# Optimization experiments

Hardware: AMD Instinct MI355X
Metric: run time of the kernel (lower is better)

The kernel has to match this reference:

```python
import jax, jax.numpy as jnp
import numpy as np

C = 256          # num_input_channels[-1]
D_REC = 256      # recog_feature_depth
B = 4            # regions (pages)
R = 1024         # boxes per region
N = B * R
T_REC = 16
K = 32           # self.k: 1 self slot + K-1 neighbors
D_MODEL = 256    # 2 * initial_depth
N_HEADS = 8
D_FF = 512
N_LAYERS = 4
SEM_DIM = 113    # initial_depth - 1 - pos_channels(14)
EPS = 1e-5


def _bn1d(x, g, b):
    # eval-mode BatchNorm, running mean 0 / var 1
    return x * (g / jnp.sqrt(1.0 + EPS)) + b


def _ln(x, g, b):
    m = x.mean(-1, keepdims=True)
    v = ((x - m) ** 2).mean(-1, keepdims=True)
    return (x - m) * jax.lax.rsqrt(v + EPS) * g + b


def _forward(rectified_quads, original_quads, recog_features,
             conv_w, conv_b, conv_bn_g, conv_bn_b,
             recog_w, recog_b,
             cp_w1, cp_b1, cp_bn1_g, cp_bn1_b,
             cp_w2, cp_b2, cp_bn2_g, cp_bn2_b,
             enc_wqkv, enc_bqkv, enc_wo, enc_bo,
             enc_ln1_g, enc_ln1_b, enc_ln2_g, enc_ln2_b,
             enc_w1, enc_b1, enc_w2, enc_b2,
             head_w, head_b, region_counts):
    n = rectified_quads.shape[0]
    b = region_counts.shape[0]
    r = n // b  # equal-size regions
    kn = K - 1

    quads = original_quads / 1024.0  # quad_downscale
    mid_pts = jax.lax.stop_gradient(quads.mean(axis=1))  # [N,2]

    # rect_proj: 1x1 conv + eval BN2d + ReLU, averaged over the 2x3 grid
    h = jnp.einsum('oc,nchw->nohw', conv_w, rectified_quads) + conv_b[None, :, None, None]
    h = jax.nn.relu(h * (conv_bn_g / jnp.sqrt(1.0 + EPS))[None, :, None, None] + conv_bn_b[None, :, None, None])
    avg_rects = h.reshape(n, C, -1).sum(axis=2) / 6.0  # num_valid_pos = g_w*g_h

    recog_enc = (jax.lax.stop_gradient(recog_features) @ recog_w.T + recog_b).mean(axis=1)

    sem = jnp.concatenate([avg_rects, recog_enc], axis=1)
    sem = jax.nn.relu(_bn1d(sem @ cp_w1.T + cp_b1, cp_bn1_g, cp_bn1_b))
    sem = jax.nn.relu(_bn1d(sem @ cp_w2.T + cp_b2, cp_bn2_g, cp_bn2_b))  # [N,113]

    h1 = quads[:, 3] - quads[:, 0]
    h2 = quads[:, 2] - quads[:, 1]
    d1 = (quads[:, 1] + h2 / 2) - (quads[:, 0] + h1 / 2)
    wdth = jnp.linalg.norm(d1, axis=1, keepdims=True)
    d1 = d1 / jnp.maximum(wdth, 1e-6)
    hts = jnp.linalg.norm((h1 + h2) / 2, axis=1, keepdims=True)
    d2 = jnp.stack([-d1[:, 1], d1[:, 0]], axis=-1)
    full_enc = jnp.concatenate([sem, quads.reshape(n, 8), d1, d2, wdth, hts], axis=1)  # [N,127]

    rects = full_enc.reshape(b, r, -1)
    centers = mid_pts.reshape(b, r, 2)
    qds = quads.reshape(b, r, 4, 2)

    def region(cr, cc, cq):
        # kNN by quad-center euclidean distance, self excluded
        qc = cq.mean(axis=1)  # [r,2]
        sq = ((qc[:, None] - qc[None, :]) ** 2).sum(-1)
        eye = jnp.eye(r, dtype=bool)
        dist = jnp.sqrt(jnp.where(eye, 1.0, sq))
        dist = jnp.where(eye, jnp.inf, dist)
        negd, idx = jax.lax.top_k(-dist, kn)  # kn smallest
        nd = -negd                             # [r,kn]
        to_rects = cr[idx]                     # [r,kn,127]
        to_centers = cc[idx]                   # [r,kn,2]

        # cosine direction features (detached in the original)
        cqs = jax.lax.stop_gradient(cq)
        tcs = jax.lax.stop_gradient(to_centers)
        pt0 = (cqs[:, 0] + cqs[:, 3]) / 2
        pt1 = (cqs[:, 1] + cqs[:, 2]) / 2
        dr = pt1 - pt0
        dr = dr / jnp.maximum(jnp.linalg.norm(dr, axis=1, keepdims=True), 1e-6)
        ctr = (pt0 + pt1) / 2
        vec = tcs - ctr[:, None]
        vec = vec / jnp.maximum(jnp.linalg.norm(vec, axis=2, keepdims=True), 1e-6)
        cosang = jnp.einsum('fv,ftv->ft', dr, vec)  # [r,kn]

        to_rects = jnp.concatenate([jnp.zeros((r, 1, to_rects.shape[-1]), to_rects.dtype), to_rects], axis=1)
        dists = jnp.concatenate([jnp.full((r, 1), -1.0, nd.dtype), nd], axis=1)
        dirs = jnp.concatenate([jnp.full((r, 1), -2.0, cosang.dtype), cosang], axis=1)
        to_feat = jnp.concatenate([to_rects, dists[..., None], dirs[..., None]], axis=2)  # [r,K,129]
        from_feat = jnp.broadcast_to(cr[:, None, :], (r, K, cr.shape[-1]))
        enc_in = jnp.concatenate([from_feat, to_feat], axis=2)  # [r,K,256]
        idx_full = jnp.concatenate([jnp.zeros((r, 1), idx.dtype), idx + 1], axis=1)  # [r,K]
        return enc_in, idx_full

    enc_in, idx_full = jax.vmap(region)(rects, centers, qds)

    # pre-norm TransformerEncoder (eval: no dropout) + Linear(dim, 3)
    x = enc_in.reshape(b * r, K, D_MODEL)
    dh = D_MODEL // N_HEADS
    for i in range(N_LAYERS):
        y = _ln(x, enc_ln1_g[i], enc_ln1_b[i])
        qkv = y @ enc_wqkv[i].T + enc_bqkv[i]
        q, k_, v = jnp.split(qkv, 3, axis=-1)
        q = q.reshape(-1, K, N_HEADS, dh).transpose(0, 2, 1, 3)
        k_ = k_.reshape(-1, K, N_HEADS, dh).transpose(0, 2, 1, 3)
        v = v.reshape(-1, K, N_HEADS, dh).transpose(0, 2, 1, 3)
        att = jax.nn.softmax(jnp.einsum('nhqd,nhkd->nhqk', q, k_) / jnp.sqrt(jnp.float32(dh)), axis=-1)
        o = jnp.einsum('nhqk,nhkd->nhqd', att, v).transpose(0, 2, 1, 3).reshape(-1, K, D_MODEL)
        x = x + o @ enc_wo[i].T + enc_bo[i]
        y = _ln(x, enc_ln2_g[i], enc_ln2_b[i])
        x = x + jax.nn.relu(y @ enc_w1[i].T + enc_b1[i]) @ enc_w2[i].T + enc_b2[i]
    dots = (x @ head_w.T + head_b).reshape(b, r, K, 3).transpose(0, 3, 1, 2)  # [b,3,r,K]

    # prohibit_self_connection: scatter into a -inf [r, r+1] relation matrix
    rows = jnp.arange(r)[:, None]

    def scat(dv, iv):
        out = jnp.full((3, r, r + 1), -jnp.inf, dv.dtype)
        return out.at[:, rows, iv].set(dv)

    # [b,3,r,r+1]: channel 0=words, 1=lines, 2=line_log_var_unc
    return jax.vmap(scat)(dots, idx_full)


def setup_inputs() -> dict:
    key = jax.random.key(0)
    ks = jax.random.split(key, 64)
    it = iter(range(64))

    def rn(shape, s=0.05):
        return jax.random.normal(ks[next(it)], shape, jnp.float32) * s

    inp = {}
    inp['rectified_quads'] = jax.random.normal(ks[next(it)], (N, C, 2, 3), jnp.float32)
    inp['original_quads'] = jax.random.uniform(ks[next(it)], (N, 4, 2), jnp.float32) * 1024.0
    inp['recog_features'] = jax.random.normal(ks[next(it)], (N, T_REC, D_REC), jnp.float32)
    inp['conv_w'] = rn((C, C)); inp['conv_b'] = rn((C,))
    inp['conv_bn_g'] = 1.0 + rn((C,)); inp['conv_bn_b'] = rn((C,))
    inp['recog_w'] = rn((C, D_REC)); inp['recog_b'] = rn((C,))
    inp['cp_w1'] = rn((2 * C, 2 * C)); inp['cp_b1'] = rn((2 * C,))
    inp['cp_bn1_g'] = 1.0 + rn((2 * C,)); inp['cp_bn1_b'] = rn((2 * C,))
    inp['cp_w2'] = rn((SEM_DIM, 2 * C)); inp['cp_b2'] = rn((SEM_DIM,))
    inp['cp_bn2_g'] = 1.0 + rn((SEM_DIM,)); inp['cp_bn2_b'] = rn((SEM_DIM,))
    L = N_LAYERS
    inp['enc_wqkv'] = rn((L, 3 * D_MODEL, D_MODEL)); inp['enc_bqkv'] = rn((L, 3 * D_MODEL))
    inp['enc_wo'] = rn((L, D_MODEL, D_MODEL)); inp['enc_bo'] = rn((L, D_MODEL))
    inp['enc_ln1_g'] = jnp.ones((L, D_MODEL)); inp['enc_ln1_b'] = jnp.zeros((L, D_MODEL))
    inp['enc_ln2_g'] = jnp.ones((L, D_MODEL)); inp['enc_ln2_b'] = jnp.zeros((L, D_MODEL))
    inp['enc_w1'] = rn((L, D_FF, D_MODEL)); inp['enc_b1'] = rn((L, D_FF))
    inp['enc_w2'] = rn((L, D_MODEL, D_FF)); inp['enc_b2'] = rn((L, D_MODEL))
    inp['head_w'] = rn((3, D_MODEL)); inp['head_b'] = rn((3,))
    inp['region_counts'] = jnp.full((B,), R, dtype=jnp.int32)
    return inp


def reference(rectified_quads, original_quads, recog_features,
              conv_w, conv_b, conv_bn_g, conv_bn_b,
              recog_w, recog_b,
              cp_w1, cp_b1, cp_bn1_g, cp_bn1_b,
              cp_w2, cp_b2, cp_bn2_g, cp_bn2_b,
              enc_wqkv, enc_bqkv, enc_wo, enc_bo,
              enc_ln1_g, enc_ln1_b, enc_ln2_g, enc_ln2_b,
              enc_w1, enc_b1, enc_w2, enc_b2,
              head_w, head_b, region_counts):
    return _forward(rectified_quads, original_quads, recog_features,
                    conv_w, conv_b, conv_bn_g, conv_bn_b,
                    recog_w, recog_b,
                    cp_w1, cp_b1, cp_bn1_g, cp_bn1_b,
                    cp_w2, cp_b2, cp_bn2_g, cp_bn2_b,
                    enc_wqkv, enc_bqkv, enc_wo, enc_bo,
                    enc_ln1_g, enc_ln1_b, enc_ln2_g, enc_ln2_b,
                    enc_w1, enc_b1, enc_w2, enc_b2,
                    head_w, head_b, region_counts)
```

## Files before the change

### kernel.cpp

```cpp
#include <hip/hip_runtime.h>
#include <cmath>

#define KN    31
#define EPSV  1e-5f
#define NEG_BIG -1.0e30f

typedef unsigned short u16;
typedef unsigned long long u64;
typedef __attribute__((ext_vector_type(8))) short bf16x8_t;
typedef __attribute__((ext_vector_type(4))) float f32x4_t;

#define LDS_FENCE() asm volatile("s_waitcnt lgkmcnt(0)" ::: "memory")

__device__ __forceinline__ u16 f2bf(float f) {
  unsigned u = __float_as_uint(f);
  u += 0x7fffu + ((u >> 16) & 1u);
  return (u16)(u >> 16);
}

__global__ void k_cvt(const float* __restrict__ src, u16* __restrict__ dst, int n) {
  int i = blockIdx.x * blockDim.x + threadIdx.x;
  if (i < n) dst[i] = f2bf(src[i]);
}

__global__ __launch_bounds__(256) void k_rect(const float* __restrict__ rq,
    const float* __restrict__ w, const float* __restrict__ cb,
    const float* __restrict__ g, const float* __restrict__ bb,
    float* __restrict__ concat) {
  __shared__ float xs[1536];
  int n = blockIdx.x, t = threadIdx.x;
  const float* src = rq + (size_t)n * 1536;
  for (int i = t; i < 1536; i += 256) xs[i] = src[i];
  __syncthreads();
  float acc[6] = {0, 0, 0, 0, 0, 0};
  const float* wr = w + (size_t)t * 256;
  for (int c = 0; c < 256; c++) {
    float wv = wr[c];
#pragma unroll
    for (int p = 0; p < 6; p++) acc[p] += wv * xs[c * 6 + p];
  }
  float scale = g[t] / sqrtf(1.f + EPSV);
  float sh = bb[t], cbv = cb[t];
  float s = 0.f;
#pragma unroll
  for (int p = 0; p < 6; p++) {
    float v = (acc[p] + cbv) * scale + sh;
    s += fmaxf(v, 0.f);
  }
  concat[(size_t)n * 512 + t] = s * (1.f / 6.f);
}

__global__ __launch_bounds__(256) void k_recog(const float* __restrict__ rf,
    const float* __restrict__ w, const float* __restrict__ b,
    float* __restrict__ concat) {
  __shared__ float tmp[256];
  int n = blockIdx.x, t = threadIdx.x;
  const float* src = rf + (size_t)n * 4096;
  float s = 0.f;
  for (int tt = 0; tt < 16; tt++) s += src[tt * 256 + t];
  tmp[t] = s * (1.f / 16.f);
  __syncthreads();
  const float* wr = w + (size_t)t * 256;
  float d = b[t];
  for (int c = 0; c < 256; c++) d += wr[c] * tmp[c];
  concat[(size_t)n * 512 + 256 + t] = d;
}

__global__ __launch_bounds__(256) void k_sem(const float* __restrict__ concat,
    const float* __restrict__ w1, const float* __restrict__ b1,
    const float* __restrict__ g1, const float* __restrict__ s1,
    const float* __restrict__ w2, const float* __restrict__ b2,
    const float* __restrict__ g2, const float* __restrict__ s2,
    float* __restrict__ fe) {
  __shared__ float in4[4][512];
  __shared__ float h1[4][512];
  int n0 = blockIdx.x * 4, t = threadIdx.x;
  for (int i = t; i < 2048; i += 256) in4[i >> 9][i & 511] = concat[(size_t)n0 * 512 + i];
  __syncthreads();
#pragma unroll
  for (int rep = 0; rep < 2; rep++) {
    int o = t + rep * 256;
    float a0 = 0, a1 = 0, a2 = 0, a3 = 0;
    const float* wr = w1 + (size_t)o * 512;
    for (int k = 0; k < 512; k++) {
      float wv = wr[k];
      a0 += wv * in4[0][k]; a1 += wv * in4[1][k];
      a2 += wv * in4[2][k]; a3 += wv * in4[3][k];
    }
    float sc = g1[o] / sqrtf(1.f + EPSV), sh = s1[o], bi = b1[o];
    h1[0][o] = fmaxf((a0 + bi) * sc + sh, 0.f);
    h1[1][o] = fmaxf((a1 + bi) * sc + sh, 0.f);
    h1[2][o] = fmaxf((a2 + bi) * sc + sh, 0.f);
    h1[3][o] = fmaxf((a3 + bi) * sc + sh, 0.f);
  }
  __syncthreads();
  if (t < 113) {
    const float* wr = w2 + (size_t)t * 512;
    float sc = g2[t] / sqrtf(1.f + EPSV), sh = s2[t], bi = b2[t];
    for (int bb = 0; bb < 4; bb++) {
      float a = 0.f;
      for (int k = 0; k < 512; k++) a += wr[k] * h1[bb][k];
      fe[(size_t)(n0 + bb) * 127 + t] = fmaxf((a + bi) * sc + sh, 0.f);
    }
  }
}

__global__ void k_geom(const float* __restrict__ oq, float* __restrict__ fe,
                       float* __restrict__ qc) {
  int n = blockIdx.x * blockDim.x + threadIdx.x;
  if (n >= 4096) return;
  const float* q = oq + (size_t)n * 8;
  float p[8];
#pragma unroll
  for (int i = 0; i < 8; i++) p[i] = q[i] * (1.f / 1024.f);
  float cx = __fadd_rn(__fadd_rn(__fadd_rn(p[0], p[2]), p[4]), p[6]) * 0.25f;
  float cy = __fadd_rn(__fadd_rn(__fadd_rn(p[1], p[3]), p[5]), p[7]) * 0.25f;
  qc[n * 2] = cx; qc[n * 2 + 1] = cy;
  float h1x = p[6] - p[0], h1y = p[7] - p[1];
  float h2x = p[4] - p[2], h2y = p[5] - p[3];
  float d1x = (p[2] + h2x * 0.5f) - (p[0] + h1x * 0.5f);
  float d1y = (p[3] + h2y * 0.5f) - (p[1] + h1y * 0.5f);
  float wd = sqrtf(d1x * d1x + d1y * d1y);
  float iw = 1.f / fmaxf(wd, 1e-6f);
  d1x *= iw; d1y *= iw;
  float mx = (h1x + h2x) * 0.5f, my = (h1y + h2y) * 0.5f;
  float ht = sqrtf(mx * mx + my * my);
  float* o = fe + (size_t)n * 127 + 113;
  o[0] = p[0]; o[1] = p[1]; o[2] = p[2]; o[3] = p[3];
  o[4] = p[4]; o[5] = p[5]; o[6] = p[6]; o[7] = p[7];
  o[8] = d1x; o[9] = d1y; o[10] = -d1y; o[11] = d1x;
  o[12] = wd; o[13] = ht;
}

__global__ __launch_bounds__(64) void k_knn(const float* __restrict__ qc,
    const float* __restrict__ oq,
    int* __restrict__ nidx, float* __restrict__ ndist, float* __restrict__ ncos) {
  int gb = blockIdx.x;
  int b = gb >> 10, fl = gb & 1023;
  int l = threadIdx.x;
  const float* qcr = qc + (size_t)b * 2048;
  const float2* qc2 = (const float2*)qcr;
  float fx = qcr[fl * 2], fy = qcr[fl * 2 + 1];
  u64 key[16];
#pragma unroll
  for (int m = 0; m < 16; m++) {
    int j = l + 64 * m;
    float2 c = qc2[j];
    float dx = __fsub_rn(fx, c.x);
    float dy = __fsub_rn(fy, c.y);
    float sq = __fadd_rn(__fmul_rn(dx, dx), __fmul_rn(dy, dy));
    float d = sqrtf(sq);
    key[m] = ((u64)__float_as_uint(d) << 32) | (unsigned)j;
    if (j == fl) key[m] = ~0ull;
  }
  unsigned my_idx = 0; float my_d = 0.f;
  for (int s = 0; s < KN; s++) {
    u64 mk = ~0ull; int mi = 0;
#pragma unroll
    for (int m = 0; m < 16; m++) if (key[m] < mk) { mk = key[m]; mi = m; }
    u64 rk = mk;
#pragma unroll
    for (int off = 1; off < 64; off <<= 1) {
      u64 o = __shfl_xor(rk, off);
      if (o < rk) rk = o;
    }
    if (mk == rk) key[mi] = ~0ull;
    if (s == l) { my_idx = (unsigned)(rk & 0xffffffffu); my_d = __uint_as_float((unsigned)(rk >> 32)); }
  }
  if (l < KN) {
    const float* q = oq + (size_t)gb * 8;
    float p0x = q[0] * (1.f / 1024.f), p0y = q[1] * (1.f / 1024.f);
    float p1x = q[2] * (1.f / 1024.f), p1y = q[3] * (1.f / 1024.f);
    float p2x = q[4] * (1.f / 1024.f), p2y = q[5] * (1.f / 1024.f);
    float p3x = q[6] * (1.f / 1024.f), p3y = q[7] * (1.f / 1024.f);
    float pt0x = (p0x + p3x) * 0.5f, pt0y = (p0y + p3y) * 0.5f;
    float pt1x = (p1x + p2x) * 0.5f, pt1y = (p1y + p2y) * 0.5f;
    float drx = pt1x - pt0x, dry = pt1y - pt0y;
    float dn = sqrtf(drx * drx + dry * dry);
    float idn = 1.f / fmaxf(dn, 1e-6f);
    drx *= idn; dry *= idn;
    float ctrx = (pt0x + pt1x) * 0.5f, ctry = (pt0y + pt1y) * 0.5f;
    float2 nc = qc2[my_idx];
    float vx = nc.x - ctrx, vy = nc.y - ctry;
    float nv = sqrtf(vx * vx + vy * vy);
    float inv = 1.f / fmaxf(nv, 1e-6f);
    ncos[(size_t)gb * KN + l] = drx * (vx * inv) + dry * (vy * inv);
    ndist[(size_t)gb * KN + l] = my_d;
    nidx[(size_t)gb * KN + l] = (int)my_idx;
  }
}

__global__ __launch_bounds__(256) void k_build(const float* __restrict__ fe,
    const int* __restrict__ nidx, const float* __restrict__ ndist,
    const float* __restrict__ ncos, float* __restrict__ x) {
  __shared__ float self[127];
  int f = blockIdx.x, t = threadIdx.x;
  if (t < 127) self[t] = fe[(size_t)f * 127 + t];
  __syncthreads();
  int base = f & ~1023;
  float* xr = x + (size_t)f * 32 * 256;
  for (int s = 0; s < 32; s++) {
    float v;
    if (t < 127) v = self[t];
    else if (t < 254) {
      int c = t - 127;
      if (s == 0) v = 0.f;
      else {
        int nb = base + nidx[(size_t)f * KN + s - 1];
        v = fe[(size_t)nb * 127 + c];
      }
    } else if (t == 254) v = (s == 0) ? -1.f : ndist[(size_t)f * KN + s - 1];
    else                 v = (s == 0) ? -2.f : ncos[(size_t)f * KN + s - 1];
    xr[s * 256 + t] = v;
  }
}

#define AFRS 520
__global__ __launch_bounds__(256, 2) void k_xf(
    float* __restrict__ x,
    const u16* __restrict__ wqkv_b, const float* __restrict__ bqkv,
    const u16* __restrict__ wo_b,  const float* __restrict__ bo,
    const float* __restrict__ l1g, const float* __restrict__ l1b,
    const float* __restrict__ l2g, const float* __restrict__ l2b,
    const u16* __restrict__ w1_b,  const float* __restrict__ b1,
    const u16* __restrict__ w2_b,  const float* __restrict__ b2) {
  __shared__ u16 afr[32 * AFRS];
  __shared__ union {
    u16 scr[4][2560];
    u16 mfr[32 * AFRS];
    float ores[64][132];
  } uu;
  int t = threadIdx.x;
  int w = t >> 6, l = t & 63;
  int ln15 = l & 15, lg4 = l >> 4;
  int r = t >> 3, c8 = t & 7;
  float* xg = x + (size_t)blockIdx.x * 64 * 256;

  float xv[2][32];
#pragma unroll
  for (int b = 0; b < 2; b++)
#pragma unroll
    for (int u4 = 0; u4 < 8; u4++) {
      float4 v4 = ((const float4*)(xg + (b * 32 + r) * 256 + c8 * 32))[u4];
      xv[b][u4 * 4 + 0] = v4.x; xv[b][u4 * 4 + 1] = v4.y;
      xv[b][u4 * 4 + 2] = v4.z; xv[b][u4 * 4 + 3] = v4.w;
    }

  const float iss = 0.17677669529663687f;

  auto ln_afr = [&](const float* gg, const float* bb) {
#pragma unroll
    for (int b = 0; b < 2; b++) {
      float s = 0.f, q = 0.f;
#pragma unroll
      for (int i = 0; i < 32; i++) { s += xv[b][i]; q += xv[b][i] * xv[b][i]; }
      s += __shfl_xor(s, 1); q += __shfl_xor(q, 1);
      s += __shfl_xor(s, 2); q += __shfl_xor(q, 2);
      s += __shfl_xor(s, 4); q += __shfl_xor(q, 4);
      float mean = s * (1.f / 256.f);
      float var = q * (1.f / 256.f) - mean * mean;
      float rstd = rsqrtf(fmaxf(var, 0.f) + EPSV);
      int k0 = c8 * 32;
      unsigned pk[16];
#pragma unroll
      for (int i2 = 0; i2 < 16; i2++) {
        float y0 = (xv[b][2 * i2] - mean) * rstd * gg[k0 + 2 * i2] + bb[k0 + 2 * i2];
        float y1 = (xv[b][2 * i2 + 1] - mean) * rstd * gg[k0 + 2 * i2 + 1] + bb[k0 + 2 * i2 + 1];
        pk[i2] = (unsigned)f2bf(y0) | ((unsigned)f2bf(y1) << 16);
      }
      int mt = b * 2 + (r >> 4);
#pragma unroll
      for (int g = 0; g < 4; g++)
        *(uint4*)&afr[(c8 * 4 + mt) * AFRS + ((r & 15) + 16 * g) * 8] =
            make_uint4(pk[g * 4 + 0], pk[g * 4 + 1], pk[g * 4 + 2], pk[g * 4 + 3]);
    }
  };

#pragma unroll 1
  for (int L = 0; L < 4; L++) {
    const u16* wqkv = wqkv_b + (size_t)L * 768 * 256;
    const float* bq = bqkv + L * 768;
    const u16* wo = wo_b + (size_t)L * 256 * 256;
    const float* bov_ = bo + L * 256;
    const float* g1 = l1g + L * 256; const float* be1 = l1b + L * 256;
    const float* g2 = l2g + L * 256; const float* be2 = l2b + L * 256;
    const u16* w1 = w1_b + (size_t)L * 512 * 256; const float* bb1 = b1 + L * 512;
    const u16* w2 = w2_b + (size_t)L * 256 * 512; const float* bb2 = b2 + L * 256;

    auto chunk256 = [&](const u16* wbase, int wrow, f32x4_t acc[4][2]) {
      const u16* wb = wbase + ((size_t)(wrow + ln15) * 256 + lg4 * 8);
#pragma unroll
      for (int kf = 0; kf < 8; kf++) {
        bf16x8_t b0 = *(const bf16x8_t*)(wb + kf * 32);
        bf16x8_t b1 = *(const bf16x8_t*)(wb + 16 * 256 + kf * 32);
#pragma unroll
        for (int mt = 0; mt < 4; mt++) {
          bf16x8_t a = *(bf16x8_t*)&afr[(kf * 4 + mt) * AFRS + l * 8];
          acc[mt][0] = __builtin_amdgcn_mfma_f32_16x16x32_bf16(a, b0, acc[mt][0], 0, 0, 0);
          acc[mt][1] = __builtin_amdgcn_mfma_f32_16x16x32_bf16(a, b1, acc[mt][1], 0, 0, 0);
        }
      }
    };

    ln_afr(g1, be1);
    __syncthreads();

    u16* sp = uu.scr[w];
    unsigned po[32];

#pragma unroll
    for (int hh = 0; hh < 2; hh++) {
      int h = 2 * w + hh;
      bf16x8_t qa[2][2], kb[2][2], vb[2][2];
      {
        f32x4_t acc[4][2] = {{{}, {}}, {{}, {}}, {{}, {}}, {{}, {}}};
        chunk256(wqkv, h * 32, acc);
#pragma unroll
        for (int mt = 0; mt < 4; mt++)
#pragma unroll
          for (int n = 0; n < 2; n++) {
            float bias = bq[h * 32 + n * 16 + ln15];
#pragma unroll
            for (int rg = 0; rg < 4; rg++)
              sp[(mt * 16 + lg4 * 4 + rg) * 40 + n * 16 + ln15] = f2bf(acc[mt][n][rg] + bias);
          }
        LDS_FENCE();
#pragma unroll
        for (int b = 0; b < 2; b++)
#pragma unroll
          for (int m = 0; m < 2; m++)
            qa[b][m] = *(const bf16x8_t*)&sp[(b * 32 + m * 16 + ln15) * 40 + lg4 * 8];
        asm volatile("" ::: "memory");
      }
      {
        f32x4_t acc[4][2] = {{{}, {}}, {{}, {}}, {{}, {}}, {{}, {}}};
        chunk256(wqkv, 256 + h * 32, acc);
#pragma unroll
        for (int mt = 0; mt < 4; mt++)
#pragma unroll
          for (int n = 0; n < 2; n++) {
            float bias = bq[256 + h * 32 + n * 16 + ln15];
#pragma unroll
            for (int rg = 0; rg < 4; rg++)
              sp[(mt * 16 + lg4 * 4 + rg) * 40 + n * 16 + ln15] = f2bf(acc[mt][n][rg] + bias);
          }
        LDS_FENCE();
#pragma unroll
        for (int b = 0; b < 2; b++)
#pragma unroll
          for (int n = 0; n < 2; n++)
            kb[b][n] = *(const bf16x8_t*)&sp[(b * 32 + n * 16 + ln15) * 40 + lg4 * 8];
        asm volatile("" ::: "memory");
      }
      {
        f32x4_t acc[4][2] = {{{}, {}}, {{}, {}}, {{}, {}}, {{}, {}}};
        chunk256(wqkv, 512 + h * 32, acc);
#pragma unroll
        for (int mt = 0; mt < 4; mt++)
#pragma unroll
          for (int n = 0; n < 2; n++) {
            float bias = bq[512 + h * 32 + n * 16 + ln15];
            int b = mt >> 1;
            int d = n * 16 + ln15;
#pragma unroll
            for (int rg = 0; rg < 4; rg++) {
              int tok = (mt & 1) * 16 + lg4 * 4 + rg;
              sp[(b * 32 + d) * 40 + tok] = f2bf(acc[mt][n][rg] + bias);
            }
          }
        LDS_FENCE();
#pragma unroll
        for (int b = 0; b < 2; b++)
#pragma unroll
          for (int n = 0; n < 2; n++)
            vb[b][n] = *(const bf16x8_t*)&sp[(b * 32 + n * 16 + ln15) * 40 + lg4 * 8];
        asm volatile("" ::: "memory");
      }
#pragma unroll
      for (int b = 0; b < 2; b++) {
        f32x4_t s00 = {}, s01 = {}, s10 = {}, s11 = {};
        s00 = __builtin_amdgcn_mfma_f32_16x16x32_bf16(qa[b][0], kb[b][0], s00, 0, 0, 0);
        s01 = __builtin_amdgcn_mfma_f32_16x16x32_bf16(qa[b][0], kb[b][1], s01, 0, 0, 0);
        s10 = __builtin_amdgcn_mfma_f32_16x16x32_bf16(qa[b][1], kb[b][0], s10, 0, 0, 0);
        s11 = __builtin_amdgcn_mfma_f32_16x16x32_bf16(qa[b][1], kb[b][1], s11, 0, 0, 0);
#pragma unroll
        for (int m = 0; m < 2; m++) {
          const f32x4_t& sv0 = m ? s10 : s00;
          const f32x4_t& sv1 = m ? s11 : s01;
#pragma unroll
          for (int rg = 0; rg < 4; rg++) {
            float v0 = sv0[rg] * iss, v1 = sv1[rg] * iss;
            float mx = fmaxf(v0, v1);
            mx = fmaxf(mx, __shfl_xor(mx, 1));
            mx = fmaxf(mx, __shfl_xor(mx, 2));
            mx = fmaxf(mx, __shfl_xor(mx, 4));
            mx = fmaxf(mx, __shfl_xor(mx, 8));
            float e0 = __expf(v0 - mx), e1 = __expf(v1 - mx);
            float sm = e0 + e1;
            sm += __shfl_xor(sm, 1);
            sm += __shfl_xor(sm, 2);
            sm += __shfl_xor(sm, 4);
            sm += __shfl_xor(sm, 8);
            float inv = 1.f / sm;
            int rr = m * 16 + lg4 * 4 + rg;
            sp[(b * 32 + rr) * 40 + ln15] = f2bf(e0 * inv);
            sp[(b * 32 + rr) * 40 + 16 + ln15] = f2bf(e1 * inv);
          }
        }
        LDS_FENCE();
        bf16x8_t pa[2];
#pragma unroll
        for (int m = 0; m < 2; m++)
          pa[m] = *(const bf16x8_t*)&sp[(b * 32 + m * 16 + ln15) * 40 + lg4 * 8];
        asm volatile("" ::: "memory");
        f32x4_t o00 = {}, o01 = {}, o10 = {}, o11 = {};
        o00 = __builtin_amdgcn_mfma_f32_16x16x32_bf16(pa[0], vb[b][0], o00, 0, 0, 0);
        o01 = __builtin_amdgcn_mfma_f32_16x16x32_bf16(pa[0], vb[b][1], o01, 0, 0, 0);
        o10 = __builtin_amdgcn_mfma_f32_16x16x32_bf16(pa[1], vb[b][0], o10, 0, 0, 0);
        o11 = __builtin_amdgcn_mfma_f32_16x16x32_bf16(pa[1], vb[b][1], o11, 0, 0, 0);
#pragma unroll
        for (int m = 0; m < 2; m++)
#pragma unroll
          for (int n = 0; n < 2; n++) {
            const f32x4_t& ov = m ? (n ? o11 : o10) : (n ? o01 : o00);
            int base = ((hh * 2 + b) * 4 + m * 2 + n) * 2;
            po[base + 0] = (unsigned)f2bf(ov[0]) | ((unsigned)f2bf(ov[1]) << 16);
            po[base + 1] = (unsigned)f2bf(ov[2]) | ((unsigned)f2bf(ov[3]) << 16);
          }
      }
    }
    __syncthreads();

#pragma unroll
    for (int hh = 0; hh < 2; hh++) {
      int h = 2 * w + hh;
#pragma unroll
      for (int b = 0; b < 2; b++)
#pragma unroll
        for (int m = 0; m < 2; m++)
#pragma unroll
          for (int n = 0; n < 2; n++) {
            int base = ((hh * 2 + b) * 4 + m * 2 + n) * 2;
            int lp = 16 * (n * 2 + (ln15 >> 3));
            int e = ln15 & 7;
#pragma unroll
            for (int rg = 0; rg < 4; rg++) {
              unsigned pv = po[base + (rg >> 1)];
              u16 v = (rg & 1) ? (u16)(pv >> 16) : (u16)(pv & 0xffff);
              afr[(h * 4 + b * 2 + m) * AFRS + ((lg4 * 4 + rg) + lp) * 8 + e] = v;
            }
          }
    }
    __syncthreads();

#pragma unroll
    for (int half = 0; half < 2; half++) {
      f32x4_t acc[4][2] = {{{}, {}}, {{}, {}}, {{}, {}}, {{}, {}}};
      chunk256(wo, (w + 4 * half) * 32, acc);
      __syncthreads();
#pragma unroll
      for (int mt = 0; mt < 4; mt++)
#pragma unroll
        for (int n = 0; n < 2; n++) {
          int col = (w + 4 * half) * 32 + n * 16 + ln15;
          float bvv = bov_[col];
#pragma unroll
          for (int rg = 0; rg < 4; rg++)
            uu.ores[mt * 16 + lg4 * 4 + rg][w * 32 + n * 16 + ln15] = acc[mt][n][rg] + bvv;
        }
      __syncthreads();
      if ((c8 >> 2) == half) {
#pragma unroll
        for (int b = 0; b < 2; b++) {
          const float* orow = &uu.ores[b * 32 + r][(c8 & 3) * 32];
#pragma unroll
          for (int u4 = 0; u4 < 8; u4++) {
            float4 v4 = *(const float4*)(orow + u4 * 4);
            xv[b][u4 * 4 + 0] += v4.x; xv[b][u4 * 4 + 1] += v4.y;
            xv[b][u4 * 4 + 2] += v4.z; xv[b][u4 * 4 + 3] += v4.w;
          }
        }
      }
      __syncthreads();
    }

    ln_afr(g2, be2);
    __syncthreads();

    f32x4_t facc[2][4][2];
#pragma unroll
    for (int i = 0; i < 2; i++)
#pragma unroll
      for (int mt = 0; mt < 4; mt++)
#pragma unroll
        for (int n = 0; n < 2; n++) facc[i][mt][n] = (f32x4_t){};

#pragma unroll
    for (int half = 0; half < 2; half++) {
#pragma unroll
      for (int ii = 0; ii < 2; ii++) {
        int c = w + 4 * (2 * half + ii);
        f32x4_t acc[4][2] = {{{}, {}}, {{}, {}}, {{}, {}}, {{}, {}}};
        chunk256(w1, c * 32, acc);
#pragma unroll
        for (int n = 0; n < 2; n++) {
          int col = c * 32 + n * 16 + ln15;
          float bv = bb1[col];
          int kf2 = (col >> 5) & 7, g = (col >> 3) & 3, e = col & 7;
#pragma unroll
          for (int mt = 0; mt < 4; mt++)
#pragma unroll
            for (int rg = 0; rg < 4; rg++) {
              int row0 = lg4 * 4 + rg;
              uu.mfr[(kf2 * 4 + mt) * AFRS + (row0 + 16 * g) * 8 + e] =
                  f2bf(fmaxf(acc[mt][n][rg] + bv, 0.f));
            }
        }
      }
      __syncthreads();
#pragma unroll
      for (int i2 = 0; i2 < 2; i2++) {
        const u16* wb = w2 + ((size_t)((w + 4 * i2) * 32 + ln15) * 512 + lg4 * 8 + half * 256);
#pragma unroll
        for (int kf = 0; kf < 8; kf++) {
          bf16x8_t b0 = *(const bf16x8_t*)(wb + kf * 32);
          bf16x8_t b1 = *(const bf16x8_t*)(wb + 16 * 512 + kf * 32);
#pragma unroll
          for (int mt = 0; mt < 4; mt++) {
            bf16x8_t a = *(bf16x8_t*)&uu.mfr[(kf * 4 + mt) * AFRS + l * 8];
            facc[i2][mt][0] = __builtin_amdgcn_mfma_f32_16x16x32_bf16(a, b0, facc[i2][mt][0], 0, 0, 0);
            facc[i2][mt][1] = __builtin_amdgcn_mfma_f32_16x16x32_bf16(a, b1, facc[i2][mt][1], 0, 0, 0);
          }
        }
      }
      __syncthreads();
    }

#pragma unroll
    for (int half = 0; half < 2; half++) {
#pragma unroll
      for (int mt = 0; mt < 4; mt++)
#pragma unroll
        for (int n = 0; n < 2; n++) {
          int col = (w + 4 * half) * 32 + n * 16 + ln15;
          float bvv = bb2[col];
#pragma unroll
          for (int rg = 0; rg < 4; rg++)
            uu.ores[mt * 16 + lg4 * 4 + rg][w * 32 + n * 16 + ln15] = facc[half][mt][n][rg] + bvv;
        }
      __syncthreads();
      if ((c8 >> 2) == half) {
#pragma unroll
        for (int b = 0; b < 2; b++) {
          const float* orow = &uu.ores[b * 32 + r][(c8 & 3) * 32];
#pragma unroll
          for (int u4 = 0; u4 < 8; u4++) {
            float4 v4 = *(const float4*)(orow + u4 * 4);
            xv[b][u4 * 4 + 0] += v4.x; xv[b][u4 * 4 + 1] += v4.y;
            xv[b][u4 * 4 + 2] += v4.z; xv[b][u4 * 4 + 3] += v4.w;
          }
        }
      }
      __syncthreads();
    }
  }

#pragma unroll
  for (int b = 0; b < 2; b++)
#pragma unroll
    for (int u4 = 0; u4 < 8; u4++) {
      float4 v4 = make_float4(xv[b][u4 * 4 + 0], xv[b][u4 * 4 + 1],
                              xv[b][u4 * 4 + 2], xv[b][u4 * 4 + 3]);
      ((float4*)(xg + (b * 32 + r) * 256 + c8 * 32))[u4] = v4;
    }
}

__global__ void k_fill(float* __restrict__ out, int n4) {
  int i = blockIdx.x * blockDim.x + threadIdx.x;
  if (i < n4) {
    float4 v = make_float4(NEG_BIG, NEG_BIG, NEG_BIG, NEG_BIG);
    ((float4*)out)[i] = v;
  }
}

__global__ __launch_bounds__(256) void k_head(const float* __restrict__ x,
    const float* __restrict__ hw, const float* __restrict__ hb,
    const int* __restrict__ nidx, float* __restrict__ out) {
  __shared__ float xr[32][260];
  __shared__ int cols[32];
  int f = blockIdx.x, t = threadIdx.x;
  const float* xg = x + (size_t)f * 32 * 256;
  for (int r = 0; r < 32; r++) xr[r][t] = xg[r * 256 + t];
  if (t < 32) cols[t] = (t == 0) ? 0 : (nidx[(size_t)f * KN + t - 1] + 1);
  __syncthreads();
  if (t < 96) {
    int s = t / 3, ch = t % 3;
    const float* wr = hw + ch * 256;
    float a = hb[ch];
    for (int c = 0; c < 256; c++) a += wr[c] * xr[s][c];
    int b = f >> 10, fl = f & 1023;
    out[(((size_t)(b * 3 + ch)) * 1024 + fl) * 1025 + cols[s]] = a;
  }
}

extern "C" void kernel_launch(void* const* d_in, const int* in_sizes, int n_in,
                              void* d_out, int out_size, void* d_ws, size_t ws_size,
                              hipStream_t stream) {
  const float* rq      = (const float*)d_in[0];
  const float* oq      = (const float*)d_in[1];
  const float* rf      = (const float*)d_in[2];
  const float* conv_w  = (const float*)d_in[3];
  const float* conv_b  = (const float*)d_in[4];
  const float* conv_g  = (const float*)d_in[5];
  const float* conv_bb = (const float*)d_in[6];
  const float* recog_w = (const float*)d_in[7];
  const float* recog_b = (const float*)d_in[8];
  const float* cp_w1   = (const float*)d_in[9];
  const float* cp_b1   = (const float*)d_in[10];
  const float* cp_g1   = (const float*)d_in[11];
  const float* cp_s1   = (const float*)d_in[12];
  const float* cp_w2   = (const float*)d_in[13];
  const float* cp_b2   = (const float*)d_in[14];
  const float* cp_g2   = (const float*)d_in[15];
  const float* cp_s2   = (const float*)d_in[16];
  const float* wqkv    = (const float*)d_in[17];
  const float* bqkv    = (const float*)d_in[18];
  const float* wo      = (const float*)d_in[19];
  const float* bo      = (const float*)d_in[20];
  const float* l1g     = (const float*)d_in[21];
  const float* l1b     = (const float*)d_in[22];
  const float* l2g     = (const float*)d_in[23];
  const float* l2b     = (const float*)d_in[24];
  const float* w1      = (const float*)d_in[25];
  const float* b1      = (const float*)d_in[26];
  const float* w2      = (const float*)d_in[27];
  const float* b2      = (const float*)d_in[28];
  const float* hw      = (const float*)d_in[29];
  const float* hb      = (const float*)d_in[30];
  float* out = (float*)d_out;

  char* ws = (char*)d_ws;
  size_t off = 0;
  auto alloc = [&](size_t bytes) { void* p = ws + off; off += (bytes + 255) & ~(size_t)255; return p; };
  float* concat = (float*)alloc(4096ull * 512 * 4);
  float* fe     = (float*)alloc(4096ull * 127 * 4);
  float* qc     = (float*)alloc(4096ull * 2 * 4);
  int*   nidx   = (int*)alloc(4096ull * KN * 4);
  float* ndist  = (float*)alloc(4096ull * KN * 4);
  float* ncos   = (float*)alloc(4096ull * KN * 4);
  float* x      = (float*)alloc(4096ull * 32 * 256 * 4);
  u16* wqkv_b   = (u16*)alloc(4ull * 768 * 256 * 2);
  u16* wo_b     = (u16*)alloc(4ull * 256 * 256 * 2);
  u16* w1_b     = (u16*)alloc(4ull * 512 * 256 * 2);
  u16* w2_b     = (u16*)alloc(4ull * 256 * 512 * 2);
  (void)in_sizes; (void)n_in; (void)out_size; (void)ws_size;

  k_cvt<<<(4 * 768 * 256 + 255) / 256, 256, 0, stream>>>(wqkv, wqkv_b, 4 * 768 * 256);
  k_cvt<<<(4 * 256 * 256 + 255) / 256, 256, 0, stream>>>(wo, wo_b, 4 * 256 * 256);
  k_cvt<<<(4 * 512 * 256 + 255) / 256, 256, 0, stream>>>(w1, w1_b, 4 * 512 * 256);
  k_cvt<<<(4 * 256 * 512 + 255) / 256, 256, 0, stream>>>(w2, w2_b, 4 * 256 * 512);

  int n4 = (4 * 3 * 1024 * 1025) / 4;
  k_fill<<<(n4 + 255) / 256, 256, 0, stream>>>(out, n4);
  k_rect<<<4096, 256, 0, stream>>>(rq, conv_w, conv_b, conv_g, conv_bb, concat);
  k_recog<<<4096, 256, 0, stream>>>(rf, recog_w, recog_b, concat);
  k_sem<<<1024, 256, 0, stream>>>(concat, cp_w1, cp_b1, cp_g1, cp_s1,
                                  cp_w2, cp_b2, cp_g2, cp_s2, fe);
  k_geom<<<16, 256, 0, stream>>>(oq, fe, qc);
  k_knn<<<4096, 64, 0, stream>>>(qc, oq, nidx, ndist, ncos);
  k_build<<<4096, 256, 0, stream>>>(fe, nidx, ndist, ncos, x);
  k_xf<<<2048, 256, 0, stream>>>(x, wqkv_b, bqkv, wo_b, bo,
                                 l1g, l1b, l2g, l2b, w1_b, b1, w2_b, b2);
  k_head<<<4096, 256, 0, stream>>>(x, hw, hb, nidx, out);
}
```

Before: 2.189 ms.

## Run transformer block with 512 threads, one head per wave, bf16 residual staging

New measurement: 2.182 ms. No clear change (-0.3%).

```diff
diff --git a/kernel.cpp b/kernel.cpp
--- a/kernel.cpp
+++ b/kernel.cpp
@@ -17,6 +17,8 @@
   u += 0x7fffu + ((u >> 16) & 1u);
   return (u16)(u >> 16);
 }
+__device__ __forceinline__ float bflo(unsigned u) { return __uint_as_float(u << 16); }
+__device__ __forceinline__ float bfhi(unsigned u) { return __uint_as_float(u & 0xffff0000u); }
 
 __global__ void k_cvt(const float* __restrict__ src, u16* __restrict__ dst, int n) {
   int i = blockIdx.x * blockDim.x + threadIdx.x;
@@ -216,7 +218,7 @@
 }
 
 #define AFRS 520
-__global__ __launch_bounds__(256, 2) void k_xf(
+__global__ __launch_bounds__(512, 4) void k_xf(
     float* __restrict__ x,
     const u16* __restrict__ wqkv_b, const float* __restrict__ bqkv,
     const u16* __restrict__ wo_b,  const float* __restrict__ bo,
@@ -226,9 +228,9 @@
     const u16* __restrict__ w2_b,  const float* __restrict__ b2) {
   __shared__ u16 afr[32 * AFRS];
   __shared__ union {
-    u16 scr[4][2560];
+    u16 scr[8][2560];
     u16 mfr[32 * AFRS];
-    float ores[64][132];
+    u16 oresb[64 * 264];
   } uu;
   int t = threadIdx.x;
   int w = t >> 6, l = t & 63;
@@ -236,44 +238,39 @@
   int r = t >> 3, c8 = t & 7;
   float* xg = x + (size_t)blockIdx.x * 64 * 256;
 
-  float xv[2][32];
-#pragma unroll
-  for (int b = 0; b < 2; b++)
-#pragma unroll
-    for (int u4 = 0; u4 < 8; u4++) {
-      float4 v4 = ((const float4*)(xg + (b * 32 + r) * 256 + c8 * 32))[u4];
-      xv[b][u4 * 4 + 0] = v4.x; xv[b][u4 * 4 + 1] = v4.y;
-      xv[b][u4 * 4 + 2] = v4.z; xv[b][u4 * 4 + 3] = v4.w;
-    }
+  float xv[32];
+#pragma unroll
+  for (int u4 = 0; u4 < 8; u4++) {
+    float4 v4 = ((const float4*)(xg + r * 256 + c8 * 32))[u4];
+    xv[u4 * 4 + 0] = v4.x; xv[u4 * 4 + 1] = v4.y;
+    xv[u4 * 4 + 2] = v4.z; xv[u4 * 4 + 3] = v4.w;
+  }
 
   const float iss = 0.17677669529663687f;
 
   auto ln_afr = [&](const float* gg, const float* bb) {
-#pragma unroll
-    for (int b = 0; b < 2; b++) {
-      float s = 0.f, q = 0.f;
-#pragma unroll
-      for (int i = 0; i < 32; i++) { s += xv[b][i]; q += xv[b][i] * xv[b][i]; }
-      s += __shfl_xor(s, 1); q += __shfl_xor(q, 1);
-      s += __shfl_xor(s, 2); q += __shfl_xor(q, 2);
-      s += __shfl_xor(s, 4); q += __shfl_xor(q, 4);
-      float mean = s * (1.f / 256.f);
-      float var = q * (1.f / 256.f) - mean * mean;
-      float rstd = rsqrtf(fmaxf(var, 0.f) + EPSV);
-      int k0 = c8 * 32;
-      unsigned pk[16];
-#pragma unroll
-      for (int i2 = 0; i2 < 16; i2++) {
-        float y0 = (xv[b][2 * i2] - mean) * rstd * gg[k0 + 2 * i2] + bb[k0 + 2 * i2];
-        float y1 = (xv[b][2 * i2 + 1] - mean) * rstd * gg[k0 + 2 * i2 + 1] + bb[k0 + 2 * i2 + 1];
-        pk[i2] = (unsigned)f2bf(y0) | ((unsigned)f2bf(y1) << 16);
-      }
-      int mt = b * 2 + (r >> 4);
-#pragma unroll
-      for (int g = 0; g < 4; g++)
-        *(uint4*)&afr[(c8 * 4 + mt) * AFRS + ((r & 15) + 16 * g) * 8] =
-            make_uint4(pk[g * 4 + 0], pk[g * 4 + 1], pk[g * 4 + 2], pk[g * 4 + 3]);
-    }
+    float s = 0.f, q = 0.f;
+#pragma unroll
+    for (int i = 0; i < 32; i++) { s += xv[i]; q += xv[i] * xv[i]; }
+    s += __shfl_xor(s, 1); q += __shfl_xor(q, 1);
+    s += __shfl_xor(s, 2); q += __shfl_xor(q, 2);
+    s += __shfl_xor(s, 4); q += __shfl_xor(q, 4);
+    float mean = s * (1.f / 256.f);
+    float var = q * (1.f / 256.f) - mean * mean;
+    float rstd = rsqrtf(fmaxf(var, 0.f) + EPSV);
+    int k0 = c8 * 32;
+    unsigned pk[16];
+#pragma unroll
+    for (int i2 = 0; i2 < 16; i2++) {
+      float y0 = (xv[2 * i2] - mean) * rstd * gg[k0 + 2 * i2] + bb[k0 + 2 * i2];
+      float y1 = (xv[2 * i2 + 1] - mean) * rstd * gg[k0 + 2 * i2 + 1] + bb[k0 + 2 * i2 + 1];
+      pk[i2] = (unsigned)f2bf(y0) | ((unsigned)f2bf(y1) << 16);
+    }
+    int mt = r >> 4;
+#pragma unroll
+    for (int g = 0; g < 4; g++)
+      *(uint4*)&afr[(c8 * 4 + mt) * AFRS + ((r & 15) + 16 * g) * 8] =
+          make_uint4(pk[g * 4 + 0], pk[g * 4 + 1], pk[g * 4 + 2], pk[g * 4 + 3]);
   };
 
 #pragma unroll 1
@@ -306,200 +303,185 @@
     __syncthreads();
 
     u16* sp = uu.scr[w];
-    unsigned po[32];
-
-#pragma unroll
-    for (int hh = 0; hh < 2; hh++) {
-      int h = 2 * w + hh;
-      bf16x8_t qa[2][2], kb[2][2], vb[2][2];
+    unsigned po[16];
+    int h = w;
+    bf16x8_t qa[2][2], kb[2][2], vb[2][2];
+    {
+      f32x4_t acc[4][2] = {{{}, {}}, {{}, {}}, {{}, {}}, {{}, {}}};
+      chunk256(wqkv, h * 32, acc);
+#pragma unroll
+      for (int mt = 0; mt < 4; mt++)
+#pragma unroll
+        for (int n = 0; n < 2; n++) {
+          float bias = bq[h * 32 + n * 16 + ln15];
+#pragma unroll
+          for (int rg = 0; rg < 4; rg++)
+            sp[(mt * 16 + lg4 * 4 + rg) * 40 + n * 16 + ln15] = f2bf(acc[mt][n][rg] + bias);
+        }
+      LDS_FENCE();
+#pragma unroll
+      for (int b = 0; b < 2; b++)
+#pragma unroll
+        for (int m = 0; m < 2; m++)
+          qa[b][m] = *(const bf16x8_t*)&sp[(b * 32 + m * 16 + ln15) * 40 + lg4 * 8];
+      asm volatile("" ::: "memory");
+    }
+    {
+      f32x4_t acc[4][2] = {{{}, {}}, {{}, {}}, {{}, {}}, {{}, {}}};
+      chunk256(wqkv, 256 + h * 32, acc);
+#pragma unroll
+      for (int mt = 0; mt < 4; mt++)
+#pragma unroll
+        for (int n = 0; n < 2; n++) {
+          float bias = bq[256 + h * 32 + n * 16 + ln15];
+#pragma unroll
+          for (int rg = 0; rg < 4; rg++)
+            sp[(mt * 16 + lg4 * 4 + rg) * 40 + n * 16 + ln15] = f2bf(acc[mt][n][rg] + bias);
+        }
+      LDS_FENCE();
+#pragma unroll
+      for (int b = 0; b < 2; b++)
+#pragma unroll
+        for (int n = 0; n < 2; n++)
+          kb[b][n] = *(const bf16x8_t*)&sp[(b * 32 + n * 16 + ln15) * 40 + lg4 * 8];
+      asm volatile("" ::: "memory");
+    }
+    {
+      f32x4_t acc[4][2] = {{{}, {}}, {{}, {}}, {{}, {}}, {{}, {}}};
+      chunk256(wqkv, 512 + h * 32, acc);
+#pragma unroll
+      for (int mt = 0; mt < 4; mt++)
+#pragma unroll
+        for (int n = 0; n < 2; n++) {
+          float bias = bq[512 + h * 32 + n * 16 + ln15];
+          int b = mt >> 1;
+          int d = n * 16 + ln15;
+#pragma unroll
+          for (int rg = 0; rg < 4; rg++) {
+            int tok = (mt & 1) * 16 + lg4 * 4 + rg;
+            sp[(b * 32 + d) * 40 + tok] = f2bf(acc[mt][n][rg] + bias);
+          }
+        }
+      LDS_FENCE();
+#pragma unroll
+      for (int b = 0; b < 2; b++)
+#pragma unroll
+        for (int n = 0; n < 2; n++)
+          vb[b][n] = *(const bf16x8_t*)&sp[(b * 32 + n * 16 + ln15) * 40 + lg4 * 8];
+      asm volatile("" ::: "memory");
+    }
+#pragma unroll
+    for (int b = 0; b < 2; b++) {
+      f32x4_t s00 = {}, s01 = {}, s10 = {}, s11 = {};
+      s00 = __builtin_amdgcn_mfma_f32_16x16x32_bf16(qa[b][0], kb[b][0], s00, 0, 0, 0);
+      s01 = __builtin_amdgcn_mfma_f32_16x16x32_bf16(qa[b][0], kb[b][1], s01, 0, 0, 0);
+      s10 = __builtin_amdgcn_mfma_f32_16x16x32_bf16(qa[b][1], kb[b][0], s10, 0, 0, 0);
+      s11 = __builtin_amdgcn_mfma_f32_16x16x32_bf16(qa[b][1], kb[b][1], s11, 0, 0, 0);
+#pragma unroll
+      for (int m = 0; m < 2; m++) {
+        const f32x4_t& sv0 = m ? s10 : s00;
+        const f32x4_t& sv1 = m ? s11 : s01;
+#pragma unroll
+        for (int rg = 0; rg < 4; rg++) {
+          float v0 = sv0[rg] * iss, v1 = sv1[rg] * iss;
+          float mx = fmaxf(v0, v1);
+          mx = fmaxf(mx, __shfl_xor(mx, 1));
+          mx = fmaxf(mx, __shfl_xor(mx, 2));
+          mx = fmaxf(mx, __shfl_xor(mx, 4));
+          mx = fmaxf(mx, __shfl_xor(mx, 8));
+          float e0 = __expf(v0 - mx), e1 = __expf(v1 - mx);
+          float sm = e0 + e1;
+          sm += __shfl_xor(sm, 1);
+          sm += __shfl_xor(sm, 2);
+          sm += __shfl_xor(sm, 4);
+          sm += __shfl_xor(sm, 8);
+          float inv = 1.f / sm;
+          int rr = m * 16 + lg4 * 4 + rg;
+          sp[(b * 32 + rr) * 40 + ln15] = f2bf(e0 * inv);
+          sp[(b * 32 + rr) * 40 + 16 + ln15] = f2bf(e1 * inv);
+        }
+      }
+      LDS_FENCE();
+      bf16x8_t pa[2];
+#pragma unroll
+      for (int m = 0; m < 2; m++)
+        pa[m] = *(const bf16x8_t*)&sp[(b * 32 + m * 16 + ln15) * 40 + lg4 * 8];
+      asm volatile("" ::: "memory");
+      f32x4_t o00 = {}, o01 = {}, o10 = {}, o11 = {};
+      o00 = __builtin_amdgcn_mfma_f32_16x16x32_bf16(pa[0], vb[b][0], o00, 0, 0, 0);
+      o01 = __builtin_amdgcn_mfma_f32_16x16x32_bf16(pa[0], vb[b][1], o01, 0, 0, 0);
+      o10 = __builtin_amdgcn_mfma_f32_16x16x32_bf16(pa[1], vb[b][0], o10, 0, 0, 0);
+      o11 = __builtin_amdgcn_mfma_f32_16x16x32_bf16(pa[1], vb[b][1], o11, 0, 0, 0);
+#pragma unroll
+      for (int m = 0; m < 2; m++)
+#pragma unroll
+        for (int n = 0; n < 2; n++) {
+          const f32x4_t& ov = m ? (n ? o11 : o10) : (n ? o01 : o00);
+          int base = (b * 4 + m * 2 + n) * 2;
+          po[base + 0] = (unsigned)f2bf(ov[0]) | ((unsigned)f2bf(ov[1]) << 16);
+          po[base + 1] = (unsigned)f2bf(ov[2]) | ((unsigned)f2bf(ov[3]) << 16);
+        }
+    }
+    __syncthreads();
+
+#pragma unroll
+    for (int b = 0; b < 2; b++)
+#pragma unroll
+      for (int m = 0; m < 2; m++)
+#pragma unroll
+        for (int n = 0; n < 2; n++) {
+          int base = (b * 4 + m * 2 + n) * 2;
+          int lp = 16 * (n * 2 + (ln15 >> 3));
+          int e = ln15 & 7;
+#pragma unroll
+          for (int rg = 0; rg < 4; rg++) {
+            unsigned pv = po[base + (rg >> 1)];
+            u16 v = (rg & 1) ? (u16)(pv >> 16) : (u16)(pv & 0xffff);
+            afr[(h * 4 + b * 2 + m) * AFRS + ((lg4 * 4 + rg) + lp) * 8 + e] = v;
+          }
+        }
+    __syncthreads();
+
+    {
+      f32x4_t acc[4][2] = {{{}, {}}, {{}, {}}, {{}, {}}, {{}, {}}};
+      chunk256(wo, w * 32, acc);
+#pragma unroll
+      for (int mt = 0; mt < 4; mt++)
+#pragma unroll
+        for (int n = 0; n < 2; n++) {
+          int col = w * 32 + n * 16 + ln15;
+          float bvv = bov_[col];
+#pragma unroll
+          for (int rg = 0; rg < 4; rg++)
+            uu.oresb[(mt * 16 + lg4 * 4 + rg) * 264 + col] = f2bf(acc[mt][n][rg] + bvv);
+        }
+    }
+    __syncthreads();
+    {
+#pragma unroll
+      for (int j = 0; j < 4; j++) {
+        uint4 u = *(const uint4*)&uu.oresb[r * 264 + c8 * 32 + j * 8];
+        xv[j * 8 + 0] += bflo(u.x); xv[j * 8 + 1] += bfhi(u.x);
+        xv[j * 8 + 2] += bflo(u.y); xv[j * 8 + 3] += bfhi(u.y);
+        xv[j * 8 + 4] += bflo(u.z); xv[j * 8 + 5] += bfhi(u.z);
+        xv[j * 8 + 6] += bflo(u.w); xv[j * 8 + 7] += bfhi(u.w);
+      }
+    }
+    __syncthreads();
+
+    ln_afr(g2, be2);
+    __syncthreads();
+
+    f32x4_t facc[4][2];
+#pragma unroll
+    for (int mt = 0; mt < 4; mt++)
+#pragma unroll
+      for (int n = 0; n < 2; n++) facc[mt][n] = (f32x4_t){};
+
+#pragma unroll
+    for (int half = 0; half < 2; half++) {
       {
-        f32x4_t acc[4][2] = {{{}, {}}, {{}, {}}, {{}, {}}, {{}, {}}};
-        chunk256(wqkv, h * 32, acc);
-#pragma unroll
-        for (int mt = 0; mt < 4; mt++)
-#pragma unroll
-          for (int n = 0; n < 2; n++) {
-            float bias = bq[h * 32 + n * 16 + ln15];
-#pragma unroll
-            for (int rg = 0; rg < 4; rg++)
-              sp[(mt * 16 + lg4 * 4 + rg) * 40 + n * 16 + ln15] = f2bf(acc[mt][n][rg] + bias);
-          }
-        LDS_FENCE();
-#pragma unroll
-        for (int b = 0; b < 2; b++)
-#pragma unroll
-          for (int m = 0; m < 2; m++)
-            qa[b][m] = *(const bf16x8_t*)&sp[(b * 32 + m * 16 + ln15) * 40 + lg4 * 8];
-        asm volatile("" ::: "memory");
-      }
-      {
-        f32x4_t acc[4][2] = {{{}, {}}, {{}, {}}, {{}, {}}, {{}, {}}};
-        chunk256(wqkv, 256 + h * 32, acc);
-#pragma unroll
-        for (int mt = 0; mt < 4; mt++)
-#pragma unroll
-          for (int n = 0; n < 2; n++) {
-            float bias = bq[256 + h * 32 + n * 16 + ln15];
-#pragma unroll
-            for (int rg = 0; rg < 4; rg++)
-              sp[(mt * 16 + lg4 * 4 + rg) * 40 + n * 16 + ln15] = f2bf(acc[mt][n][rg] + bias);
-          }
-        LDS_FENCE();
-#pragma unroll
-        for (int b = 0; b < 2; b++)
-#pragma unroll
-          for (int n = 0; n < 2; n++)
-            kb[b][n] = *(const bf16x8_t*)&sp[(b * 32 + n * 16 + ln15) * 40 + lg4 * 8];
-        asm volatile("" ::: "memory");
-      }
-      {
-        f32x4_t acc[4][2] = {{{}, {}}, {{}, {}}, {{}, {}}, {{}, {}}};
-        chunk256(wqkv, 512 + h * 32, acc);
-#pragma unroll
-        for (int mt = 0; mt < 4; mt++)
-#pragma unroll
-          for (int n = 0; n < 2; n++) {
-            float bias = bq[512 + h * 32 + n * 16 + ln15];
-            int b = mt >> 1;
-            int d = n * 16 + ln15;
-#pragma unroll
-            for (int rg = 0; rg < 4; rg++) {
-              int tok = (mt & 1) * 16 + lg4 * 4 + rg;
-              sp[(b * 32 + d) * 40 + tok] = f2bf(acc[mt][n][rg] + bias);
-            }
-          }
-        LDS_FENCE();
-#pragma unroll
-        for (int b = 0; b < 2; b++)
-#pragma unroll
-          for (int n = 0; n < 2; n++)
-            vb[b][n] = *(const bf16x8_t*)&sp[(b * 32 + n * 16 + ln15) * 40 + lg4 * 8];
-        asm volatile("" ::: "memory");
-      }
-#pragma unroll
-      for (int b = 0; b < 2; b++) {
-        f32x4_t s00 = {}, s01 = {}, s10 = {}, s11 = {};
-        s00 = __builtin_amdgcn_mfma_f32_16x16x32_bf16(qa[b][0], kb[b][0], s00, 0, 0, 0);
-        s01 = __builtin_amdgcn_mfma_f32_16x16x32_bf16(qa[b][0], kb[b][1], s01, 0, 0, 0);
-        s10 = __builtin_amdgcn_mfma_f32_16x16x32_bf16(qa[b][1], kb[b][0], s10, 0, 0, 0);
-        s11 = __builtin_amdgcn_mfma_f32_16x16x32_bf16(qa[b][1], kb[b][1], s11, 0, 0, 0);
-#pragma unroll
-        for (int m = 0; m < 2; m++) {
-          const f32x4_t& sv0 = m ? s10 : s00;
-          const f32x4_t& sv1 = m ? s11 : s01;
-#pragma unroll
-          for (int rg = 0; rg < 4; rg++) {
-            float v0 = sv0[rg] * iss, v1 = sv1[rg] * iss;
-            float mx = fmaxf(v0, v1);
-            mx = fmaxf(mx, __shfl_xor(mx, 1));
-            mx = fmaxf(mx, __shfl_xor(mx, 2));
-            mx = fmaxf(mx, __shfl_xor(mx, 4));
-            mx = fmaxf(mx, __shfl_xor(mx, 8));
-            float e0 = __expf(v0 - mx), e1 = __expf(v1 - mx);
-            float sm = e0 + e1;
-            sm += __shfl_xor(sm, 1);
-            sm += __shfl_xor(sm, 2);
-            sm += __shfl_xor(sm, 4);
-            sm += __shfl_xor(sm, 8);
-            float inv = 1.f / sm;
-            int rr = m * 16 + lg4 * 4 + rg;
-            sp[(b * 32 + rr) * 40 + ln15] = f2bf(e0 * inv);
-            sp[(b * 32 + rr) * 40 + 16 + ln15] = f2bf(e1 * inv);
-          }
-        }
-        LDS_FENCE();
-        bf16x8_t pa[2];
-#pragma unroll
-        for (int m = 0; m < 2; m++)
-          pa[m] = *(const bf16x8_t*)&sp[(b * 32 + m * 16 + ln15) * 40 + lg4 * 8];
-        asm volatile("" ::: "memory");
-        f32x4_t o00 = {}, o01 = {}, o10 = {}, o11 = {};
-        o00 = __builtin_amdgcn_mfma_f32_16x16x32_bf16(pa[0], vb[b][0], o00, 0, 0, 0);
-        o01 = __builtin_amdgcn_mfma_f32_16x16x32_bf16(pa[0], vb[b][1], o01, 0, 0, 0);
-        o10 = __builtin_amdgcn_mfma_f32_16x16x32_bf16(pa[1], vb[b][0], o10, 0, 0, 0);
-        o11 = __builtin_amdgcn_mfma_f32_16x16x32_bf16(pa[1], vb[b][1], o11, 0, 0, 0);
-#pragma unroll
-        for (int m = 0; m < 2; m++)
-#pragma unroll
-          for (int n = 0; n < 2; n++) {
-            const f32x4_t& ov = m ? (n ? o11 : o10) : (n ? o01 : o00);
-            int base = ((hh * 2 + b) * 4 + m * 2 + n) * 2;
-            po[base + 0] = (unsigned)f2bf(ov[0]) | ((unsigned)f2bf(ov[1]) << 16);
-            po[base + 1] = (unsigned)f2bf(ov[2]) | ((unsigned)f2bf(ov[3]) << 16);
-          }
-      }
-    }
-    __syncthreads();
-
-#pragma unroll
-    for (int hh = 0; hh < 2; hh++) {
-      int h = 2 * w + hh;
-#pragma unroll
-      for (int b = 0; b < 2; b++)
-#pragma unroll
-        for (int m = 0; m < 2; m++)
-#pragma unroll
-          for (int n = 0; n < 2; n++) {
-            int base = ((hh * 2 + b) * 4 + m * 2 + n) * 2;
-            int lp = 16 * (n * 2 + (ln15 >> 3));
-            int e = ln15 & 7;
-#pragma unroll
-            for (int rg = 0; rg < 4; rg++) {
-              unsigned pv = po[base + (rg >> 1)];
-              u16 v = (rg & 1) ? (u16)(pv >> 16) : (u16)(pv & 0xffff);
-              afr[(h * 4 + b * 2 + m) * AFRS + ((lg4 * 4 + rg) + lp) * 8 + e] = v;
-            }
-          }
-    }
-    __syncthreads();
-
-#pragma unroll
-    for (int half = 0; half < 2; half++) {
-      f32x4_t acc[4][2] = {{{}, {}}, {{}, {}}, {{}, {}}, {{}, {}}};
-      chunk256(wo, (w + 4 * half) * 32, acc);
-      __syncthreads();
-#pragma unroll
-      for (int mt = 0; mt < 4; mt++)
-#pragma unroll
-        for (int n = 0; n < 2; n++) {
-          int col = (w + 4 * half) * 32 + n * 16 + ln15;
-          float bvv = bov_[col];
-#pragma unroll
-          for (int rg = 0; rg < 4; rg++)
-            uu.ores[mt * 16 + lg4 * 4 + rg][w * 32 + n * 16 + ln15] = acc[mt][n][rg] + bvv;
-        }
-      __syncthreads();
-      if ((c8 >> 2) == half) {
-#pragma unroll
-        for (int b = 0; b < 2; b++) {
-          const float* orow = &uu.ores[b * 32 + r][(c8 & 3) * 32];
-#pragma unroll
-          for (int u4 = 0; u4 < 8; u4++) {
-            float4 v4 = *(const float4*)(orow + u4 * 4);
-            xv[b][u4 * 4 + 0] += v4.x; xv[b][u4 * 4 + 1] += v4.y;
-            xv[b][u4 * 4 + 2] += v4.z; xv[b][u4 * 4 + 3] += v4.w;
-          }
-        }
-      }
-      __syncthreads();
-    }
-
-    ln_afr(g2, be2);
-    __syncthreads();
-
-    f32x4_t facc[2][4][2];
-#pragma unroll
-    for (int i = 0; i < 2; i++)
-#pragma unroll
-      for (int mt = 0; mt < 4; mt++)
-#pragma unroll
-        for (int n = 0; n < 2; n++) facc[i][mt][n] = (f32x4_t){};
-
-#pragma unroll
-    for (int half = 0; half < 2; half++) {
-#pragma unroll
-      for (int ii = 0; ii < 2; ii++) {
-        int c = w + 4 * (2 * half + ii);
+        int c = half * 8 + w;
         f32x4_t acc[4][2] = {{{}, {}}, {{}, {}}, {{}, {}}, {{}, {}}};
         chunk256(w1, c * 32, acc);
 #pragma unroll
@@ -518,9 +500,8 @@
         }
       }
       __syncthreads();
-#pragma unroll
-      for (int i2 = 0; i2 < 2; i2++) {
-        const u16* wb = w2 + ((size_t)((w + 4 * i2) * 32 + ln15) * 512 + lg4 * 8 + half * 256);
+      {
+        const u16* wb = w2 + ((size_t)(w * 32 + ln15) * 512 + lg4 * 8 + half * 256);
 #pragma unroll
         for (int kf = 0; kf < 8; kf++) {
           bf16x8_t b0 = *(const bf16x8_t*)(wb + kf * 32);
@@ -528,51 +509,45 @@
 #pragma unroll
           for (int mt = 0; mt < 4; mt++) {
             bf16x8_t a = *(bf16x8_t*)&uu.mfr[(kf * 4 + mt) * AFRS + l * 8];
-            facc[i2][mt][0] = __builtin_amdgcn_mfma_f32_16x16x32_bf16(a, b0, facc[i2][mt][0], 0, 0, 0);
-            facc[i2][mt][1] = __builtin_amdgcn_mfma_f32_16x16x32_bf16(a, b1, facc[i2][mt][1], 0, 0, 0);
+            facc[mt][0] = __builtin_amdgcn_mfma_f32_16x16x32_bf16(a, b0, facc[mt][0], 0, 0, 0);
+            facc[mt][1] = __builtin_amdgcn_mfma_f32_16x16x32_bf16(a, b1, facc[mt][1], 0, 0, 0);
           }
         }
       }
       __syncthreads();
     }
 
-#pragma unroll
-    for (int half = 0; half < 2; half++) {
+    {
 #pragma unroll
       for (int mt = 0; mt < 4; mt++)
 #pragma unroll
         for (int n = 0; n < 2; n++) {
-          int col = (w + 4 * half) * 32 + n * 16 + ln15;
+          int col = w * 32 + n * 16 + ln15;
           float bvv = bb2[col];
 #pragma unroll
           for (int rg = 0; rg < 4; rg++)
-            uu.ores[mt * 16 + lg4 * 4 + rg][w * 32 + n * 16 + ln15] = facc[half][mt][n][rg] + bvv;
-        }
-      __syncthreads();
-      if ((c8 >> 2) == half) {
-#pragma unroll
-        for (int b = 0; b < 2; b++) {
-          const float* orow = &uu.ores[b * 32 + r][(c8 & 3) * 32];
-#pragma unroll
-          for (int u4 = 0; u4 < 8; u4++) {
-            float4 v4 = *(const float4*)(orow + u4 * 4);
-            xv[b][u4 * 4 + 0] += v4.x; xv[b][u4 * 4 + 1] += v4.y;
-            xv[b][u4 * 4 + 2] += v4.z; xv[b][u4 * 4 + 3] += v4.w;
-          }
-        }
+            uu.oresb[(mt * 16 + lg4 * 4 + rg) * 264 + col] = f2bf(facc[mt][n][rg] + bvv);
+        }
+    }
+    __syncthreads();
+    {
+#pragma unroll
+      for (int j = 0; j < 4; j++) {
+        uint4 u = *(const uint4*)&uu.oresb[r * 264 + c8 * 32 + j * 8];
+        xv[j * 8 + 0] += bflo(u.x); xv[j * 8 + 1] += bfhi(u.x);
+        xv[j * 8 + 2] += bflo(u.y); xv[j * 8 + 3] += bfhi(u.y);
+        xv[j * 8 + 4] += bflo(u.z); xv[j * 8 + 5] += bfhi(u.z);
+        xv[j * 8 + 6] += bflo(u.w); xv[j * 8 + 7] += bfhi(u.w);
       }
-      __syncthreads();
-    }
-  }
-
-#pragma unroll
-  for (int b = 0; b < 2; b++)
-#pragma unroll
-    for (int u4 = 0; u4 < 8; u4++) {
-      float4 v4 = make_float4(xv[b][u4 * 4 + 0], xv[b][u4 * 4 + 1],
-                              xv[b][u4 * 4 + 2], xv[b][u4 * 4 + 3]);
-      ((float4*)(xg + (b * 32 + r) * 256 + c8 * 32))[u4] = v4;
-    }
+    }
+    __syncthreads();
+  }
+
+#pragma unroll
+  for (int u4 = 0; u4 < 8; u4++) {
+    float4 v4 = make_float4(xv[u4 * 4 + 0], xv[u4 * 4 + 1], xv[u4 * 4 + 2], xv[u4 * 4 + 3]);
+    ((float4*)(xg + r * 256 + c8 * 32))[u4] = v4;
+  }
 }
 
 __global__ void k_fill(float* __restrict__ out, int n4) {
@@ -669,7 +644,7 @@
   k_geom<<<16, 256, 0, stream>>>(oq, fe, qc);
   k_knn<<<4096, 64, 0, stream>>>(qc, oq, nidx, ndist, ncos);
   k_build<<<4096, 256, 0, stream>>>(fe, nidx, ndist, ncos, x);
-  k_xf<<<2048, 256, 0, stream>>>(x, wqkv_b, bqkv, wo_b, bo,
+  k_xf<<<2048, 512, 0, stream>>>(x, wqkv_b, bqkv, wo_b, bo,
                                  l1g, l1b, l2g, l2b, w1_b, b1, w2_b, b2);
   k_head<<<4096, 256, 0, stream>>>(x, hw, hb, nidx, out);
 }
```
